# Kernel tuning notes

Hardware: AMD Instinct MI355X
Metric: run time of the kernel (lower is better)

The kernel has to match this reference:

```python
import jax, jax.numpy as jnp
import numpy as np

N1 = 50000; N2 = 50000; F = 256; HID = 64; H = 8; DH = HID // H; L = 2; E = 800000


def setup_inputs() -> dict:
    key = jax.random.key(0)
    ks = jax.random.split(key, 20)
    f32 = jnp.float32
    rn = lambda k, shape, s=0.1: jax.random.normal(k, shape, dtype=f32) * s
    inp = {}
    inp['x1'] = jax.random.normal(ks[0], (N1, F), dtype=f32)
    inp['x2'] = jax.random.normal(ks[1], (N2, F), dtype=f32)
    # row 0 = source node ids, row 1 = destination node ids
    inp['edge12'] = jax.random.randint(ks[2], (2, E), 0, N2)  # n1 -> n2
    inp['edge21'] = jax.random.randint(ks[3], (2, E), 0, N1)  # n2 -> n1
    inp['w_in'] = rn(ks[4], (2, HID, F))
    inp['b_in'] = rn(ks[5], (2, HID))
    inp['kw'] = rn(ks[6], (L, 2, HID, HID)); inp['kb'] = rn(ks[7], (L, 2, HID))
    inp['qw'] = rn(ks[8], (L, 2, HID, HID)); inp['qb'] = rn(ks[9], (L, 2, HID))
    inp['vw'] = rn(ks[10], (L, 2, HID, HID)); inp['vb'] = rn(ks[11], (L, 2, HID))
    inp['aw'] = rn(ks[12], (L, 2, HID, HID)); inp['ab'] = rn(ks[13], (L, 2, HID))
    inp['skip'] = jax.random.normal(ks[14], (L, 2), dtype=f32)
    inp['a_rel'] = rn(ks[15], (L, 2, H, DH, DH), 0.3)
    inp['m_rel'] = rn(ks[16], (L, 2, H, DH, DH), 0.3)
    inp['p_rel'] = jnp.ones((L, 2, H), dtype=f32)
    return inp


def _segment_softmax(logits, seg, n):
    # logits: [E, H], seg: [E] destination ids
    m = jax.ops.segment_max(logits, seg, num_segments=n)
    e = jnp.exp(logits - m[seg])
    s = jax.ops.segment_sum(e, seg, num_segments=n)
    return e / s[seg]


def reference(x1, x2, edge12, edge21, w_in, b_in, kw, kb, qw, qb, vw, vb, aw, ab,
              skip, a_rel, m_rel, p_rel):
    scale = jnp.asarray(1.0 / np.sqrt(DH), x1.dtype)

    def kqv(h, l, t):
        k = (h @ kw[l, t].T + kb[l, t]).reshape(-1, H, DH)
        q = (h @ qw[l, t].T + qb[l, t]).reshape(-1, H, DH)
        v = (h @ vw[l, t].T + vb[l, t]).reshape(-1, H, DH)
        return k, q, v

    def message(k_src, v_src, q_dst, edge, ar, mr, pr, n_dst):
        kr = jnp.einsum('nhd,hde->nhe', k_src, ar)   # per-node relation projection
        vr = jnp.einsum('nhd,hde->nhe', v_src, mr)
        s, d = edge[0], edge[1]
        logit = jnp.einsum('ehd,ehd->eh', q_dst[d], kr[s]) * pr[None, :] * scale
        alpha = _segment_softmax(logit, d, n_dst)     # [E, H]
        out = jax.ops.segment_sum(alpha[:, :, None] * vr[s], d, num_segments=n_dst)
        return out.reshape(n_dst, HID)

    def update(o, h, l, t):
        o = jax.nn.gelu(o, approximate=False) @ aw[l, t].T + ab[l, t]
        beta = jax.nn.sigmoid(skip[l, t])
        return beta * o + (1.0 - beta) * h

    # per-node-type input Linear + ReLU stem
    h1 = jax.nn.relu(x1 @ w_in[0].T + b_in[0])
    h2 = jax.nn.relu(x2 @ w_in[1].T + b_in[1])

    outs1, outs2 = [], []
    for l in range(L):
        k1, q1, v1 = kqv(h1, l, 0)
        k2, q2, v2 = kqv(h2, l, 1)
        o2 = message(k1, v1, q2, edge12, a_rel[l, 0], m_rel[l, 0], p_rel[l, 0], h2.shape[0])
        o1 = message(k2, v2, q1, edge21, a_rel[l, 1], m_rel[l, 1], p_rel[l, 1], h1.shape[0])
        h1 = update(o1, h1, l, 0)
        h2 = update(o2, h2, l, 1)
        outs1.append(h1)
        outs2.append(h2)

    Em = jnp.concatenate(outs1, axis=1)  # [N1, HID*L]
    Ed = jnp.concatenate(outs2, axis=1)  # [N2, HID*L]
    return Em, Ed
```

## Files before the change

### kernel.cpp

```cpp
#include <hip/hip_runtime.h>
#include <hip/hip_bf16.h>
#include <hip/hip_fp8.h>
#include <math.h>

typedef __attribute__((ext_vector_type(8))) short bf16x8;
typedef __attribute__((ext_vector_type(4))) float f32x4;
typedef __attribute__((ext_vector_type(4))) unsigned int u32x4;
typedef __attribute__((ext_vector_type(4))) int i32x4;
typedef unsigned short ushort_t;
typedef unsigned char uchar_t;

#define BUCKET_SHIFT 6
#define BUCKET_CAP   64

__device__ inline short f2b(float f) {
    __hip_bfloat16 h = __float2bfloat16(f);
    return __builtin_bit_cast(short, h);
}
__device__ inline float b2f(unsigned short u) {
    return __builtin_bit_cast(float, (unsigned int)u << 16);
}
__device__ inline float blo(unsigned int w) {
    return __builtin_bit_cast(float, w << 16);
}
__device__ inline float bhi(unsigned int w) {
    return __builtin_bit_cast(float, w & 0xffff0000u);
}
__device__ inline uchar_t f2f8(float f) {
    __hip_fp8_e4m3 h(f);
    return (uchar_t)h.__x;
}
__device__ inline float f82f(unsigned int u) {
    __hip_fp8_e4m3 h;
    h.__x = (__hip_fp8_storage_t)(u & 0xff);
    return (float)h;
}

__global__ __launch_bounds__(256) void prep_kernel(
    const float* __restrict__ w_in,
    const float* __restrict__ kw, const float* __restrict__ kb,
    const float* __restrict__ qw, const float* __restrict__ qb,
    const float* __restrict__ vw, const float* __restrict__ vb,
    const float* __restrict__ aw,
    const float* __restrict__ a_rel, const float* __restrict__ m_rel,
    const float* __restrict__ p_rel,
    short* __restrict__ wstem, short* __restrict__ Wcat,
    float* __restrict__ Bcat, short* __restrict__ Awb)
{
    int bid = blockIdx.x, tid = threadIdx.x;
    if (bid >= 4) {
        int t = bid - 4;
        for (int i = tid; i < 16384; i += 256)
            wstem[t * 16384 + i] = f2b(w_in[t * 16384 + i]);
        return;
    }
    int base = bid;
    const float* KW = kw + base * 4096;
    const float* QW = qw + base * 4096;
    const float* VW = vw + base * 4096;
    const float* AR = a_rel + base * 512;
    const float* MR = m_rel + base * 512;
    const float* PR = p_rel + base * 8;
    short* WC = Wcat + base * 12288;
    float* BC = Bcat + base * 192;

    for (int i = tid; i < 4096; i += 256) WC[i] = f2b(QW[i]);
    for (int i = tid; i < 4096; i += 256) {
        int out = i >> 6, in = i & 63;
        int h = out >> 3, e = out & 7;
        float s = PR[h] * 0.35355339059327373f;
        float acc = 0.f;
        #pragma unroll
        for (int d = 0; d < 8; ++d) acc += KW[(h * 8 + d) * 64 + in] * AR[h * 64 + d * 8 + e];
        WC[4096 + i] = f2b(acc * s);
    }
    for (int i = tid; i < 4096; i += 256) {
        int out = i >> 6, in = i & 63;
        int h = out >> 3, e = out & 7;
        float acc = 0.f;
        #pragma unroll
        for (int d = 0; d < 8; ++d) acc += VW[(h * 8 + d) * 64 + in] * MR[h * 64 + d * 8 + e];
        WC[8192 + i] = f2b(acc);
    }
    if (tid < 64) {
        BC[tid] = qb[base * 64 + tid];
    } else if (tid < 128) {
        int out = tid - 64;
        int h = out >> 3, e = out & 7;
        float s = PR[h] * 0.35355339059327373f;
        float acc = 0.f;
        #pragma unroll
        for (int d = 0; d < 8; ++d) acc += kb[base * 64 + h * 8 + d] * AR[h * 64 + d * 8 + e];
        BC[64 + out] = acc * s;
    } else if (tid < 192) {
        int out = tid - 128;
        int h = out >> 3, e = out & 7;
        float acc = 0.f;
        #pragma unroll
        for (int d = 0; d < 8; ++d) acc += vb[base * 64 + h * 8 + d] * MR[h * 64 + d * 8 + e];
        BC[128 + out] = acc;
    }
    for (int i = tid; i < 4096; i += 256) Awb[base * 4096 + i] = f2b(aw[base * 4096 + i]);
}

__global__ __launch_bounds__(256) void stem2_mfma(
    const float* __restrict__ X1, const float* __restrict__ X2,
    const short* __restrict__ Wb, const float* __restrict__ B1, const float* __restrict__ B2,
    short* __restrict__ H1, short* __restrict__ H2, int N1, int N2, int nt1)
{
    const float* X; const short* Wsrc; const float* B; short* Hb; int N; int tb;
    if (blockIdx.x < nt1) { X = X1; Wsrc = Wb;         B = B1; Hb = H1; N = N1; tb = blockIdx.x; }
    else                  { X = X2; Wsrc = Wb + 16384; B = B2; Hb = H2; N = N2; tb = blockIdx.x - nt1; }
    __shared__ short Ws[64 * 256];
    int tid = threadIdx.x;
    #pragma unroll
    for (int k = 0; k < 8; ++k) {
        int u = tid + k * 256;
        int row = u >> 5, c = u & 31;
        u32x4 v = *reinterpret_cast<const u32x4*>(Wsrc + row * 256 + c * 8);
        *reinterpret_cast<u32x4*>(&Ws[row * 256 + ((c ^ (row & 7)) << 3)]) = v;
    }
    __syncthreads();
    int w = tid >> 6, l = tid & 63;
    int g = l >> 4, q = l & 15;
    int row = tb * 64 + w * 16 + q;
    bool rok = row < N;
    f32x4 acc[4] = {};
    const float* xr = X + (size_t)row * 256 + g * 8;
    #pragma unroll
    for (int s = 0; s < 8; ++s) {
        bf16x8 a = {};
        if (rok) {
            float4 x0 = *reinterpret_cast<const float4*>(xr + s * 32);
            float4 x1 = *reinterpret_cast<const float4*>(xr + s * 32 + 4);
            a[0] = f2b(x0.x); a[1] = f2b(x0.y); a[2] = f2b(x0.z); a[3] = f2b(x0.w);
            a[4] = f2b(x1.x); a[5] = f2b(x1.y); a[6] = f2b(x1.z); a[7] = f2b(x1.w);
        }
        #pragma unroll
        for (int n = 0; n < 4; ++n) {
            int br = n * 16 + q;
            int c = s * 4 + g;
            bf16x8 b = *reinterpret_cast<bf16x8*>(&Ws[br * 256 + ((c ^ (br & 7)) << 3)]);
            acc[n] = __builtin_amdgcn_mfma_f32_16x16x32_bf16(a, b, acc[n], 0, 0, 0);
        }
    }
    int orow0 = tb * 64 + w * 16 + g * 4;
    #pragma unroll
    for (int n = 0; n < 4; ++n) {
        int col = n * 16 + q;
        float bias = B[col];
        #pragma unroll
        for (int r = 0; r < 4; ++r) {
            int orow = orow0 + r;
            if (orow < N)
                Hb[(size_t)orow * 64 + col] = f2b(fmaxf(acc[n][r] + bias, 0.f));
        }
    }
}

__global__ __launch_bounds__(256) void kqv2_mfma(
    const short* __restrict__ H1, const short* __restrict__ Wc1, const float* __restrict__ Bc1,
    short* __restrict__ Q1, uchar_t* __restrict__ KV1, int N1,
    const short* __restrict__ H2, const short* __restrict__ Wc2, const float* __restrict__ Bc2,
    short* __restrict__ Q2, uchar_t* __restrict__ KV2, int N2, int nt1)
{
    const short* Hb; const short* Wcat; const float* Bcat; short* Qb; uchar_t* KV; int N; int tb;
    if (blockIdx.x < nt1) { Hb = H1; Wcat = Wc1; Bcat = Bc1; Qb = Q1; KV = KV1; N = N1; tb = blockIdx.x; }
    else                  { Hb = H2; Wcat = Wc2; Bcat = Bc2; Qb = Q2; KV = KV2; N = N2; tb = blockIdx.x - nt1; }
    __shared__ short Ws[192 * 64];
    int tid = threadIdx.x;
    #pragma unroll
    for (int k = 0; k < 6; ++k) {
        int u = tid + k * 256;
        int row = u >> 3, c = u & 7;
        u32x4 v = *reinterpret_cast<const u32x4*>(Wcat + row * 64 + c * 8);
        *reinterpret_cast<u32x4*>(&Ws[row * 64 + ((c ^ (row & 7)) << 3)]) = v;
    }
    __syncthreads();
    int w = tid >> 6, l = tid & 63;
    int g = l >> 4, q = l & 15;
    int arow = tb * 64 + w * 16 + q;
    bool rok = arow < N;
    bf16x8 a0 = {}, a1 = {};
    if (rok) {
        a0 = *reinterpret_cast<const bf16x8*>(Hb + (size_t)arow * 64 + g * 8);
        a1 = *reinterpret_cast<const bf16x8*>(Hb + (size_t)arow * 64 + 32 + g * 8);
    }
    f32x4 acc[12] = {};
    #pragma unroll
    for (int n = 0; n < 12; ++n) {
        int br = n * 16 + q;
        bf16x8 b0 = *reinterpret_cast<bf16x8*>(&Ws[br * 64 + ((0 * 4 + g) ^ (br & 7)) * 8]);
        acc[n] = __builtin_amdgcn_mfma_f32_16x16x32_bf16(a0, b0, acc[n], 0, 0, 0);
        bf16x8 b1 = *reinterpret_cast<bf16x8*>(&Ws[br * 64 + ((1 * 4 + g) ^ (br & 7)) * 8]);
        acc[n] = __builtin_amdgcn_mfma_f32_16x16x32_bf16(a1, b1, acc[n], 0, 0, 0);
    }
    int orow0 = tb * 64 + w * 16 + g * 4;
    #pragma unroll
    for (int n = 0; n < 12; ++n) {
        int col = n * 16 + q;
        float bias = Bcat[col];
        #pragma unroll
        for (int r = 0; r < 4; ++r) {
            int orow = orow0 + r;
            if (orow < N) {
                float v = acc[n][r] + bias;
                if (n < 4)      Qb[(size_t)orow * 64 + col]              = f2b(v);
                else if (n < 8) KV[(size_t)orow * 128 + 2 * (col - 64)]  = f2f8(v);
                else            KV[(size_t)orow * 128 + 2 * (col - 128) + 1] = f2f8(v);
            }
        }
    }
}

__global__ __launch_bounds__(256) void bucket8d_kernel(
    const int* __restrict__ e12, const int* __restrict__ e21,
    int* __restrict__ cnt12, int* __restrict__ cnt21,
    ushort_t* __restrict__ cs12, ushort_t* __restrict__ cs21,
    int E, int N1, int N2, int G)
{
    int grp = blockIdx.x & 7;
    int blk = blockIdx.x >> 3;
    bool dirA = grp < 4;
    const int* srcp = dirA ? e12 : e21;
    const int* dstp = dirA ? (e12 + E) : (e21 + E);
    int* cnt = dirA ? cnt12 : cnt21;
    ushort_t* cs = dirA ? cs12 : cs21;
    int Nn = dirA ? N2 : N1;
    int qr = grp & 3;
    int range = (Nn + 3) >> 2;
    int lo = qr * range, hi = lo + range;
    int E4 = E >> 2;
    int stride = G * 256;
    for (int v = blk * 256 + threadIdx.x; v < E4; v += stride) {
        i32x4 d4 = __builtin_nontemporal_load(reinterpret_cast<const i32x4*>(dstp) + v);
        int base = v * 4;
        if (d4.x >= lo && d4.x < hi) { int p = atomicAdd(&cnt[d4.x], 1); if (p < BUCKET_CAP) cs[((size_t)d4.x << BUCKET_SHIFT) + p] = (ushort_t)srcp[base]; }
        if (d4.y >= lo && d4.y < hi) { int p = atomicAdd(&cnt[d4.y], 1); if (p < BUCKET_CAP) cs[((size_t)d4.y << BUCKET_SHIFT) + p] = (ushort_t)srcp[base + 1]; }
        if (d4.z >= lo && d4.z < hi) { int p = atomicAdd(&cnt[d4.z], 1); if (p < BUCKET_CAP) cs[((size_t)d4.z << BUCKET_SHIFT) + p] = (ushort_t)srcp[base + 2]; }
        if (d4.w >= lo && d4.w < hi) { int p = atomicAdd(&cnt[d4.w], 1); if (p < BUCKET_CAP) cs[((size_t)d4.w << BUCKET_SHIFT) + p] = (ushort_t)srcp[base + 3]; }
    }
    int tail = E & 3;
    if (blk == 0 && threadIdx.x < tail) {
        int i = E - tail + threadIdx.x;
        int d = dstp[i];
        if (d >= lo && d < hi) { int p = atomicAdd(&cnt[d], 1); if (p < BUCKET_CAP) cs[((size_t)d << BUCKET_SHIFT) + p] = (ushort_t)srcp[i]; }
    }
}

__global__ __launch_bounds__(256) void gather8_kernel(
    const int* __restrict__ cntA, const ushort_t* __restrict__ csA,
    const short* __restrict__ QA, const uchar_t* __restrict__ KVA, short* __restrict__ GA, int NA,
    const int* __restrict__ cntB, const ushort_t* __restrict__ csB,
    const short* __restrict__ QB, const uchar_t* __restrict__ KVB, short* __restrict__ GB, int NB)
{
    int grp = blockIdx.x & 7;
    int localBlock = (blockIdx.x >> 3) * 4 + (grp & 3);
    const int* cnt; const ushort_t* cs; const short* Qb; const uchar_t* KV; short* G; int N;
    if (grp < 4) { cnt = cntA; cs = csA; Qb = QA; KV = KVA; G = GA; N = NA; }
    else         { cnt = cntB; cs = csB; Qb = QB; KV = KVB; G = GB; N = NB; }
    int d = localBlock * 4 + (threadIdx.x >> 6);
    if (d >= N) return;
    int lane = threadIdx.x & 63;
    int j = lane & 15;
    int sub = lane >> 4;
    int deg = min(cnt[d], BUCKET_CAP);
    uint2 qw = *reinterpret_cast<const uint2*>(Qb + (size_t)d * 64 + 4 * j);
    float q0 = blo(qw.x), q1 = bhi(qw.x), q2 = blo(qw.y), q3 = bhi(qw.y);
    float a0 = 0.f, a1 = 0.f, a2 = 0.f, a3 = 0.f, den = 0.f;
    int idv = (lane < deg) ? (int)cs[((size_t)d << BUCKET_SHIFT) + lane] : 0;
    for (int i = 0; i < deg; i += 4) {
        int idx = i + sub;
        bool valid = idx < deg;
        int s = __shfl(idv, valid ? idx : 0);
        uint2 wv = *reinterpret_cast<const uint2*>(KV + (size_t)s * 128 + 8 * j);
        float k0 = f82f(wv.x),       v0 = f82f(wv.x >> 8);
        float k1 = f82f(wv.x >> 16), v1 = f82f(wv.x >> 24);
        float k2 = f82f(wv.y),       v2 = f82f(wv.y >> 8);
        float k3 = f82f(wv.y >> 16), v3 = f82f(wv.y >> 24);
        float t = q0 * k0;
        t = fmaf(q1, k1, t);
        t = fmaf(q2, k2, t);
        t = fmaf(q3, k3, t);
        t += __shfl_xor(t, 1);
        float e = valid ? __expf(t) : 0.f;
        den += e;
        a0 = fmaf(e, v0, a0);
        a1 = fmaf(e, v1, a1);
        a2 = fmaf(e, v2, a2);
        a3 = fmaf(e, v3, a3);
    }
    a0 += __shfl_xor(a0, 16); a1 += __shfl_xor(a1, 16);
    a2 += __shfl_xor(a2, 16); a3 += __shfl_xor(a3, 16);
    den += __shfl_xor(den, 16);
    a0 += __shfl_xor(a0, 32); a1 += __shfl_xor(a1, 32);
    a2 += __shfl_xor(a2, 32); a3 += __shfl_xor(a3, 32);
    den += __shfl_xor(den, 32);
    if (lane < 16) {
        float r = (den > 0.f) ? 1.f / den : 0.f;
        float o0 = a0 * r, o1 = a1 * r, o2 = a2 * r, o3 = a3 * r;
        float g0 = 0.5f * o0 * (1.f + erff(o0 * 0.70710678118654752f));
        float g1 = 0.5f * o1 * (1.f + erff(o1 * 0.70710678118654752f));
        float g2 = 0.5f * o2 * (1.f + erff(o2 * 0.70710678118654752f));
        float g3 = 0.5f * o3 * (1.f + erff(o3 * 0.70710678118654752f));
        uint2 pw;
        pw.x = ((unsigned int)(unsigned short)f2b(g0)) | (((unsigned int)(unsigned short)f2b(g1)) << 16);
        pw.y = ((unsigned int)(unsigned short)f2b(g2)) | (((unsigned int)(unsigned short)f2b(g3)) << 16);
        *reinterpret_cast<uint2*>(G + (size_t)d * 64 + 4 * j) = pw;
    }
}

__global__ __launch_bounds__(256) void updkqv_mfma(
    const short* __restrict__ G1, const short* __restrict__ Aw1, const float* __restrict__ Ab1,
    const float* __restrict__ sk1, short* __restrict__ H1, float* __restrict__ Out1, int N1,
    const short* __restrict__ G2, const short* __restrict__ Aw2, const float* __restrict__ Ab2,
    const float* __restrict__ sk2, short* __restrict__ H2, float* __restrict__ Out2, int N2,
    const short* __restrict__ Wc1n, const float* __restrict__ Bc1n,
    short* __restrict__ Q1, uchar_t* __restrict__ KV1,
    const short* __restrict__ Wc2n, const float* __restrict__ Bc2n,
    short* __restrict__ Q2, uchar_t* __restrict__ KV2,
    int nt1, int outColOff)
{
    const short* G; const short* Awb; const float* Ab; const float* skipp;
    short* Hb; float* Out; int N; int tb;
    const short* Wcat; const float* Bcat; short* Qb; uchar_t* KV;
    if (blockIdx.x < nt1) {
        G = G1; Awb = Aw1; Ab = Ab1; skipp = sk1; Hb = H1; Out = Out1; N = N1; tb = blockIdx.x;
        Wcat = Wc1n; Bcat = Bc1n; Qb = Q1; KV = KV1;
    } else {
        G = G2; Awb = Aw2; Ab = Ab2; skipp = sk2; Hb = H2; Out = Out2; N = N2; tb = blockIdx.x - nt1;
        Wcat = Wc2n; Bcat = Bc2n; Qb = Q2; KV = KV2;
    }
    __shared__ short Ws[192 * 64];
    __shared__ short hs[64][64];
    int tid = threadIdx.x;
    #pragma unroll
    for (int k = 0; k < 6; ++k) {
        int u = tid + k * 256;
        int row = u >> 3, c = u & 7;
        u32x4 v = *reinterpret_cast<const u32x4*>(Wcat + row * 64 + c * 8);
        *reinterpret_cast<u32x4*>(&Ws[row * 64 + ((c ^ (row & 7)) << 3)]) = v;
    }
    int w = tid >> 6, l = tid & 63;
    int g = l >> 4, q = l & 15;
    bf16x8 bfw[4][2];
    #pragma unroll
    for (int n = 0; n < 4; ++n)
        #pragma unroll
        for (int s = 0; s < 2; ++s)
            bfw[n][s] = *reinterpret_cast<const bf16x8*>(Awb + (n * 16 + q) * 64 + s * 32 + g * 8);
    float beta = 1.f / (1.f + __expf(-skipp[0]));
    int arow = tb * 64 + w * 16 + q;
    bool rok = arow < N;
    bf16x8 ua0 = {}, ua1 = {};
    if (rok) {
        ua0 = *reinterpret_cast<const bf16x8*>(G + (size_t)arow * 64 + g * 8);
        ua1 = *reinterpret_cast<const bf16x8*>(G + (size_t)arow * 64 + 32 + g * 8);
    }
    f32x4 uacc[4] = {};
    #pragma unroll
    for (int n = 0; n < 4; ++n) {
        uacc[n] = __builtin_amdgcn_mfma_f32_16x16x32_bf16(ua0, bfw[n][0], uacc[n], 0, 0, 0);
        uacc[n] = __builtin_amdgcn_mfma_f32_16x16x32_bf16(ua1, bfw[n][1], uacc[n], 0, 0, 0);
    }
    int orow0 = tb * 64 + w * 16 + g * 4;
    int lrow0 = w * 16 + g * 4;
    #pragma unroll
    for (int n = 0; n < 4; ++n) {
        int col = n * 16 + q;
        float bias = Ab[col];
        #pragma unroll
        for (int r = 0; r < 4; ++r) {
            int orow = orow0 + r;
            if (orow < N) {
                float hold = b2f(((const unsigned short*)Hb)[(size_t)orow * 64 + col]);
                float hnew = beta * (uacc[n][r] + bias) + (1.f - beta) * hold;
                short hb16 = f2b(hnew);
                Out[(size_t)orow * 128 + outColOff + col] = hnew;
                Hb[(size_t)orow * 64 + col] = hb16;
                hs[lrow0 + r][col] = hb16;
            } else {
                hs[lrow0 + r][col] = 0;
            }
        }
    }
    __syncthreads();
    bf16x8 a0 = *reinterpret_cast<const bf16x8*>(&hs[w * 16 + q][g * 8]);
    bf16x8 a1 = *reinterpret_cast<const bf16x8*>(&hs[w * 16 + q][32 + g * 8]);
    f32x4 acc[12] = {};
    #pragma unroll
    for (int n = 0; n < 12; ++n) {
        int br = n * 16 + q;
        bf16x8 b0 = *reinterpret_cast<bf16x8*>(&Ws[br * 64 + ((0 * 4 + g) ^ (br & 7)) * 8]);
        acc[n] = __builtin_amdgcn_mfma_f32_16x16x32_bf16(a0, b0, acc[n], 0, 0, 0);
        bf16x8 b1 = *reinterpret_cast<bf16x8*>(&Ws[br * 64 + ((1 * 4 + g) ^ (br & 7)) * 8]);
        acc[n] = __builtin_amdgcn_mfma_f32_16x16x32_bf16(a1, b1, acc[n], 0, 0, 0);
    }
    #pragma unroll
    for (int n = 0; n < 12; ++n) {
        int col = n * 16 + q;
        float bias = Bcat[col];
        #pragma unroll
        for (int r = 0; r < 4; ++r) {
            int orow = orow0 + r;
            if (orow < N) {
                float v = acc[n][r] + bias;
                if (n < 4)      Qb[(size_t)orow * 64 + col]              = f2b(v);
                else if (n < 8) KV[(size_t)orow * 128 + 2 * (col - 64)]  = f2f8(v);
                else            KV[(size_t)orow * 128 + 2 * (col - 128) + 1] = f2f8(v);
            }
        }
    }
}

__global__ __launch_bounds__(256) void update2_mfma(
    const short* __restrict__ G1, const short* __restrict__ Aw1, const float* __restrict__ Ab1,
    const float* __restrict__ sk1, short* __restrict__ H1, float* __restrict__ Out1, int N1,
    const short* __restrict__ G2, const short* __restrict__ Aw2, const float* __restrict__ Ab2,
    const float* __restrict__ sk2, short* __restrict__ H2, float* __restrict__ Out2, int N2,
    int nt1, int outColOff)
{
    const short* G; const short* Awb; const float* Ab; const float* skipp;
    short* Hb; float* Out; int N; int tb;
    if (blockIdx.x < nt1) { G = G1; Awb = Aw1; Ab = Ab1; skipp = sk1; Hb = H1; Out = Out1; N = N1; tb = blockIdx.x; }
    else                  { G = G2; Awb = Aw2; Ab = Ab2; skipp = sk2; Hb = H2; Out = Out2; N = N2; tb = blockIdx.x - nt1; }
    int tid = threadIdx.x;
    int w = tid >> 6, l = tid & 63;
    int g = l >> 4, q = l & 15;
    bf16x8 bf[4][2];
    #pragma unroll
    for (int n = 0; n < 4; ++n)
        #pragma unroll
        for (int s = 0; s < 2; ++s)
            bf[n][s] = *reinterpret_cast<const bf16x8*>(Awb + (n * 16 + q) * 64 + s * 32 + g * 8);
    float beta = 1.f / (1.f + __expf(-skipp[0]));
    int arow = tb * 64 + w * 16 + q;
    bool rok = arow < N;
    bf16x8 a0 = {}, a1 = {};
    if (rok) {
        a0 = *reinterpret_cast<const bf16x8*>(G + (size_t)arow * 64 + g * 8);
        a1 = *reinterpret_cast<const bf16x8*>(G + (size_t)arow * 64 + 32 + g * 8);
    }
    f32x4 acc[4] = {};
    #pragma unroll
    for (int n = 0; n < 4; ++n) {
        acc[n] = __builtin_amdgcn_mfma_f32_16x16x32_bf16(a0, bf[n][0], acc[n], 0, 0, 0);
        acc[n] = __builtin_amdgcn_mfma_f32_16x16x32_bf16(a1, bf[n][1], acc[n], 0, 0, 0);
    }
    int orow0 = tb * 64 + w * 16 + g * 4;
    #pragma unroll
    for (int n = 0; n < 4; ++n) {
        int col = n * 16 + q;
        float bias = Ab[col];
        #pragma unroll
        for (int r = 0; r < 4; ++r) {
            int orow = orow0 + r;
            if (orow < N) {
                float hold = b2f(((const unsigned short*)Hb)[(size_t)orow * 64 + col]);
                float hnew = beta * (acc[n][r] + bias) + (1.f - beta) * hold;
                Out[(size_t)orow * 128 + outColOff + col] = hnew;
                Hb[(size_t)orow * 64 + col] = f2b(hnew);
            }
        }
    }
}

extern "C" void kernel_launch(void* const* d_in, const int* in_sizes, int n_in,
                              void* d_out, int out_size, void* d_ws, size_t ws_size,
                              hipStream_t stream) {
    const float* x1    = (const float*)d_in[0];
    const float* x2    = (const float*)d_in[1];
    const int*   e12   = (const int*)d_in[2];
    const int*   e21   = (const int*)d_in[3];
    const float* w_in  = (const float*)d_in[4];
    const float* b_in  = (const float*)d_in[5];
    const float* kw    = (const float*)d_in[6];
    const float* kb    = (const float*)d_in[7];
    const float* qw    = (const float*)d_in[8];
    const float* qb    = (const float*)d_in[9];
    const float* vw    = (const float*)d_in[10];
    const float* vb    = (const float*)d_in[11];
    const float* aw    = (const float*)d_in[12];
    const float* ab    = (const float*)d_in[13];
    const float* skip  = (const float*)d_in[14];
    const float* a_rel = (const float*)d_in[15];
    const float* m_rel = (const float*)d_in[16];
    const float* p_rel = (const float*)d_in[17];

    int N1 = in_sizes[0] / 256;
    int N2 = in_sizes[1] / 256;
    int E  = in_sizes[2] / 2;

    float* out = (float*)d_out;

    char* wsp = (char*)d_ws;
    auto alloc = [&](size_t bytes) { void* p = wsp; wsp += (bytes + 255) & ~(size_t)255; return p; };
    short* hb1   = (short*)alloc((size_t)N1 * 64 * 2);
    short* hb2   = (short*)alloc((size_t)N2 * 64 * 2);
    short* qb1   = (short*)alloc((size_t)N1 * 64 * 2);
    short* qb2   = (short*)alloc((size_t)N2 * 64 * 2);
    uchar_t* kv1 = (uchar_t*)alloc((size_t)N1 * 128);
    uchar_t* kv2 = (uchar_t*)alloc((size_t)N2 * 128);
    short* g1    = (short*)alloc((size_t)N1 * 64 * 2);
    short* g2    = (short*)alloc((size_t)N2 * 64 * 2);
    short* wstem = (short*)alloc(2 * 16384 * 2);
    short* WcatB = (short*)alloc(4 * 12288 * 2);
    float* BcatB = (float*)alloc(4 * 192 * 4);
    short* AwbB  = (short*)alloc(4 * 4096 * 2);
    int* cnts    = (int*)alloc((size_t)(N1 + N2) * 4);
    int* cnt12   = cnts;
    int* cnt21   = cnts + N2;
    ushort_t* csr12 = (ushort_t*)alloc(((size_t)N2 << BUCKET_SHIFT) * 2);
    ushort_t* csr21 = (ushort_t*)alloc(((size_t)N1 << BUCKET_SHIFT) * 2);

    const int BLK = 256;
    int nt1 = (N1 + 63) / 64;
    int nt2 = (N2 + 63) / 64;
    const int G8 = 512;

    prep_kernel<<<6, BLK, 0, stream>>>(w_in, kw, kb, qw, qb, vw, vb, aw,
                                       a_rel, m_rel, p_rel, wstem, WcatB, BcatB, AwbB);

    hipMemsetAsync(cnts, 0, (size_t)(N1 + N2) * 4, stream);
    bucket8d_kernel<<<8 * G8, BLK, 0, stream>>>(e12, e21, cnt12, cnt21,
                                                csr12, csr21, E, N1, N2, G8);

    stem2_mfma<<<nt1 + nt2, BLK, 0, stream>>>(x1, x2, wstem, b_in, b_in + 64,
                                              hb1, hb2, N1, N2, nt1);

    int bA = (N2 + 3) / 4;
    int bB = (N1 + 3) / 4;
    int bmax = bA > bB ? bA : bB;
    int nlb = (bmax + 3) / 4;
    int gblocks = 8 * nlb;

    kqv2_mfma<<<nt1 + nt2, BLK, 0, stream>>>(
        hb1, WcatB + (size_t)0 * 12288, BcatB + (size_t)0 * 192, qb1, kv1, N1,
        hb2, WcatB + (size_t)1 * 12288, BcatB + (size_t)1 * 192, qb2, kv2, N2, nt1);

    gather8_kernel<<<gblocks, BLK, 0, stream>>>(
        cnt12, csr12, qb2, kv1, g2, N2,
        cnt21, csr21, qb1, kv2, g1, N1);

    updkqv_mfma<<<nt1 + nt2, BLK, 0, stream>>>(
        g1, AwbB + (size_t)0 * 4096, ab + (size_t)0 * 64, skip + 0, hb1, out, N1,
        g2, AwbB + (size_t)1 * 4096, ab + (size_t)1 * 64, skip + 1, hb2,
        out + (size_t)N1 * 128, N2,
        WcatB + (size_t)2 * 12288, BcatB + (size_t)2 * 192, qb1, kv1,
        WcatB + (size_t)3 * 12288, BcatB + (size_t)3 * 192, qb2, kv2,
        nt1, 0);

    gather8_kernel<<<gblocks, BLK, 0, stream>>>(
        cnt12, csr12, qb2, kv1, g2, N2,
        cnt21, csr21, qb1, kv2, g1, N1);

    update2_mfma<<<nt1 + nt2, BLK, 0, stream>>>(
        g1, AwbB + (size_t)2 * 4096, ab + (size_t)2 * 64, skip + 2, hb1, out, N1,
        g2, AwbB + (size_t)3 * 4096, ab + (size_t)3 * 64, skip + 3, hb2,
        out + (size_t)N1 * 128, N2, nt1, 64);
}
```

Before: 302.0 us.

## Replace global-atomic edge bucketing with two-level radix binning via shared-memory atomics

The single bucketing kernel, which ran global atomics per edge across four range-partitioned passes, is replaced by a four-kernel pipeline. It builds per-block histograms of 64-node bins in LDS, scans them in a single block, scatters packed (local dst, src) payloads into bin order, and then expands each bin into the fixed-capacity per-node source lists in shared memory. This removes contended global atomics and scattered 2-byte writes, and it also drops the memset. The cost is extra kernel launches, a serial single-block scan, and an extra round trip through a payload buffer of E words per direction.

After: 353.2 us. +17.0%, slower.

```diff
diff --git a/kernel.cpp b/kernel.cpp
--- a/kernel.cpp
+++ b/kernel.cpp
@@ -12,6 +12,7 @@
 
 #define BUCKET_SHIFT 6
 #define BUCKET_CAP   64
+#define SB_ 32
 
 __device__ inline short f2b(float f) {
     __hip_bfloat16 h = __float2bfloat16(f);
@@ -213,39 +214,165 @@
     }
 }
 
-__global__ __launch_bounds__(256) void bucket8d_kernel(
+__global__ __launch_bounds__(256) void radix_hist(
     const int* __restrict__ e12, const int* __restrict__ e21,
-    int* __restrict__ cnt12, int* __restrict__ cnt21,
-    ushort_t* __restrict__ cs12, ushort_t* __restrict__ cs21,
-    int E, int N1, int N2, int G)
-{
-    int grp = blockIdx.x & 7;
-    int blk = blockIdx.x >> 3;
-    bool dirA = grp < 4;
+    int* __restrict__ histA, int* __restrict__ histB,
+    int E, int nbA, int nbB)
+{
+    int blk = blockIdx.x;
+    bool dirA = blk < SB_;
+    int b = dirA ? blk : blk - SB_;
+    const int* dstp = dirA ? (e12 + E) : (e21 + E);
+    int nb = dirA ? nbA : nbB;
+    int* hist = dirA ? histA : histB;
+    __shared__ int h[1024];
+    for (int i = threadIdx.x; i < nb; i += 256) h[i] = 0;
+    __syncthreads();
+    int EV = E >> 2;
+    int vchunk = (EV + SB_ - 1) / SB_;
+    int vs = b * vchunk, ve = min(EV, vs + vchunk);
+    for (int v = vs + threadIdx.x; v < ve; v += 256) {
+        i32x4 d4 = __builtin_nontemporal_load(reinterpret_cast<const i32x4*>(dstp) + v);
+        atomicAdd(&h[d4.x >> 6], 1);
+        atomicAdd(&h[d4.y >> 6], 1);
+        atomicAdd(&h[d4.z >> 6], 1);
+        atomicAdd(&h[d4.w >> 6], 1);
+    }
+    if (b == 0) {
+        int tail = E & 3;
+        if ((int)threadIdx.x < tail) {
+            int d = dstp[E - tail + threadIdx.x];
+            atomicAdd(&h[d >> 6], 1);
+        }
+    }
+    __syncthreads();
+    for (int i = threadIdx.x; i < nb; i += 256) hist[b * nb + i] = h[i];
+}
+
+__global__ __launch_bounds__(256) void radix_scan(
+    const int* __restrict__ histA, const int* __restrict__ histB,
+    int* __restrict__ offA, int* __restrict__ offB,
+    int* __restrict__ bsA, int* __restrict__ bsB, int nbA, int nbB)
+{
+    __shared__ int tsum[256];
+    int tid = threadIdx.x;
+    for (int dir = 0; dir < 2; ++dir) {
+        const int* hist = dir ? histB : histA;
+        int* off = dir ? offB : offA;
+        int* bs = dir ? bsB : bsA;
+        int nb = dir ? nbB : nbA;
+        int per = (nb + 255) >> 8;
+        int b0 = tid * per;
+        int loc[8];
+        int lsum = 0;
+        for (int k = 0; k < per; ++k) {
+            int b = b0 + k;
+            int t = 0;
+            if (b < nb)
+                for (int r = 0; r < SB_; ++r) t += hist[r * nb + b];
+            loc[k] = t; lsum += t;
+        }
+        __syncthreads();
+        tsum[tid] = lsum;
+        __syncthreads();
+        for (int ofs = 1; ofs < 256; ofs <<= 1) {
+            int v = (tid >= ofs) ? tsum[tid - ofs] : 0;
+            __syncthreads();
+            tsum[tid] += v;
+            __syncthreads();
+        }
+        int run = tid ? tsum[tid - 1] : 0;
+        for (int k = 0; k < per; ++k) {
+            int b = b0 + k;
+            if (b < nb) {
+                bs[b] = run;
+                int r2 = run;
+                for (int r = 0; r < SB_; ++r) {
+                    off[r * nb + b] = r2;
+                    r2 += hist[r * nb + b];
+                }
+            }
+            run += loc[k];
+        }
+        if (tid == 255) bs[nb] = tsum[255];
+        __syncthreads();
+    }
+}
+
+__global__ __launch_bounds__(256) void radix_scatter(
+    const int* __restrict__ e12, const int* __restrict__ e21,
+    const int* __restrict__ offA, const int* __restrict__ offB,
+    unsigned int* __restrict__ payA, unsigned int* __restrict__ payB,
+    int E, int nbA, int nbB)
+{
+    int blk = blockIdx.x;
+    bool dirA = blk < SB_;
+    int b = dirA ? blk : blk - SB_;
     const int* srcp = dirA ? e12 : e21;
     const int* dstp = dirA ? (e12 + E) : (e21 + E);
+    const int* off = dirA ? offA : offB;
+    unsigned int* pay = dirA ? payA : payB;
+    int nb = dirA ? nbA : nbB;
+    __shared__ int offs[1024];
+    for (int i = threadIdx.x; i < nb; i += 256) offs[i] = off[b * nb + i];
+    __syncthreads();
+    int EV = E >> 2;
+    int vchunk = (EV + SB_ - 1) / SB_;
+    int vs = b * vchunk, ve = min(EV, vs + vchunk);
+    for (int v = vs + threadIdx.x; v < ve; v += 256) {
+        i32x4 d4 = __builtin_nontemporal_load(reinterpret_cast<const i32x4*>(dstp) + v);
+        i32x4 s4 = __builtin_nontemporal_load(reinterpret_cast<const i32x4*>(srcp) + v);
+        int p;
+        p = atomicAdd(&offs[d4.x >> 6], 1); pay[p] = (((unsigned int)(d4.x & 63)) << 16) | (unsigned int)s4.x;
+        p = atomicAdd(&offs[d4.y >> 6], 1); pay[p] = (((unsigned int)(d4.y & 63)) << 16) | (unsigned int)s4.y;
+        p = atomicAdd(&offs[d4.z >> 6], 1); pay[p] = (((unsigned int)(d4.z & 63)) << 16) | (unsigned int)s4.z;
+        p = atomicAdd(&offs[d4.w >> 6], 1); pay[p] = (((unsigned int)(d4.w & 63)) << 16) | (unsigned int)s4.w;
+    }
+    if (b == 0) {
+        int tail = E & 3;
+        if ((int)threadIdx.x < tail) {
+            int i = E - tail + threadIdx.x;
+            int d = dstp[i];
+            int p = atomicAdd(&offs[d >> 6], 1);
+            pay[p] = (((unsigned int)(d & 63)) << 16) | (unsigned int)srcp[i];
+        }
+    }
+}
+
+__global__ __launch_bounds__(256) void bin_expand(
+    const unsigned int* __restrict__ payA, const int* __restrict__ bsA, int nbA,
+    ushort_t* __restrict__ cs12, int* __restrict__ cnt12, int NdA,
+    const unsigned int* __restrict__ payB, const int* __restrict__ bsB, int nbB,
+    ushort_t* __restrict__ cs21, int* __restrict__ cnt21, int NdB)
+{
+    int blk = blockIdx.x;
+    bool dirA = blk < nbA;
+    int b = dirA ? blk : blk - nbA;
+    const unsigned int* pay = dirA ? payA : payB;
+    const int* bs = dirA ? bsA : bsB;
+    ushort_t* cs = dirA ? cs12 : cs21;
     int* cnt = dirA ? cnt12 : cnt21;
-    ushort_t* cs = dirA ? cs12 : cs21;
-    int Nn = dirA ? N2 : N1;
-    int qr = grp & 3;
-    int range = (Nn + 3) >> 2;
-    int lo = qr * range, hi = lo + range;
-    int E4 = E >> 2;
-    int stride = G * 256;
-    for (int v = blk * 256 + threadIdx.x; v < E4; v += stride) {
-        i32x4 d4 = __builtin_nontemporal_load(reinterpret_cast<const i32x4*>(dstp) + v);
-        int base = v * 4;
-        if (d4.x >= lo && d4.x < hi) { int p = atomicAdd(&cnt[d4.x], 1); if (p < BUCKET_CAP) cs[((size_t)d4.x << BUCKET_SHIFT) + p] = (ushort_t)srcp[base]; }
-        if (d4.y >= lo && d4.y < hi) { int p = atomicAdd(&cnt[d4.y], 1); if (p < BUCKET_CAP) cs[((size_t)d4.y << BUCKET_SHIFT) + p] = (ushort_t)srcp[base + 1]; }
-        if (d4.z >= lo && d4.z < hi) { int p = atomicAdd(&cnt[d4.z], 1); if (p < BUCKET_CAP) cs[((size_t)d4.z << BUCKET_SHIFT) + p] = (ushort_t)srcp[base + 2]; }
-        if (d4.w >= lo && d4.w < hi) { int p = atomicAdd(&cnt[d4.w], 1); if (p < BUCKET_CAP) cs[((size_t)d4.w << BUCKET_SHIFT) + p] = (ushort_t)srcp[base + 3]; }
-    }
-    int tail = E & 3;
-    if (blk == 0 && threadIdx.x < tail) {
-        int i = E - tail + threadIdx.x;
-        int d = dstp[i];
-        if (d >= lo && d < hi) { int p = atomicAdd(&cnt[d], 1); if (p < BUCKET_CAP) cs[((size_t)d << BUCKET_SHIFT) + p] = (ushort_t)srcp[i]; }
-    }
+    int Nd = dirA ? NdA : NdB;
+    __shared__ int c[64];
+    __shared__ ushort_t list[64 * 64];
+    if (threadIdx.x < 64) c[threadIdx.x] = 0;
+    __syncthreads();
+    int rs = bs[b], re = bs[b + 1];
+    for (int i = rs + threadIdx.x; i < re; i += 256) {
+        unsigned int e = pay[i];
+        int dl = e >> 16;
+        int pos = atomicAdd(&c[dl], 1);
+        if (pos < BUCKET_CAP) list[(dl << 6) + pos] = (ushort_t)(e & 0xffff);
+    }
+    __syncthreads();
+    int d0 = b << 6;
+    int nrow = min(64, Nd - d0);
+    if (nrow <= 0) return;
+    const unsigned int* lsrc = reinterpret_cast<const unsigned int*>(list);
+    unsigned int* gdst = reinterpret_cast<unsigned int*>(cs + ((size_t)d0 << 6));
+    int nu32 = nrow << 5;
+    for (int u = threadIdx.x; u < nu32; u += 256) gdst[u] = lsrc[u];
+    if ((int)threadIdx.x < nrow) cnt[d0 + threadIdx.x] = c[threadIdx.x];
 }
 
 __global__ __launch_bounds__(256) void gather8_kernel(
@@ -507,23 +634,34 @@
     short* WcatB = (short*)alloc(4 * 12288 * 2);
     float* BcatB = (float*)alloc(4 * 192 * 4);
     short* AwbB  = (short*)alloc(4 * 4096 * 2);
-    int* cnts    = (int*)alloc((size_t)(N1 + N2) * 4);
-    int* cnt12   = cnts;
-    int* cnt21   = cnts + N2;
+    int* cnt12   = (int*)alloc((size_t)N2 * 4);
+    int* cnt21   = (int*)alloc((size_t)N1 * 4);
     ushort_t* csr12 = (ushort_t*)alloc(((size_t)N2 << BUCKET_SHIFT) * 2);
     ushort_t* csr21 = (ushort_t*)alloc(((size_t)N1 << BUCKET_SHIFT) * 2);
+
+    int nbA = (N2 + 63) >> 6;
+    int nbB = (N1 + 63) >> 6;
+    int* histA = (int*)alloc((size_t)SB_ * nbA * 4);
+    int* histB = (int*)alloc((size_t)SB_ * nbB * 4);
+    int* offA  = (int*)alloc((size_t)SB_ * nbA * 4);
+    int* offB  = (int*)alloc((size_t)SB_ * nbB * 4);
+    int* bsA   = (int*)alloc((size_t)(nbA + 1) * 4);
+    int* bsB   = (int*)alloc((size_t)(nbB + 1) * 4);
+    unsigned int* payA = (unsigned int*)alloc((size_t)E * 4);
+    unsigned int* payB = (unsigned int*)alloc((size_t)E * 4);
 
     const int BLK = 256;
     int nt1 = (N1 + 63) / 64;
     int nt2 = (N2 + 63) / 64;
-    const int G8 = 512;
 
     prep_kernel<<<6, BLK, 0, stream>>>(w_in, kw, kb, qw, qb, vw, vb, aw,
                                        a_rel, m_rel, p_rel, wstem, WcatB, BcatB, AwbB);
 
-    hipMemsetAsync(cnts, 0, (size_t)(N1 + N2) * 4, stream);
-    bucket8d_kernel<<<8 * G8, BLK, 0, stream>>>(e12, e21, cnt12, cnt21,
-                                                csr12, csr21, E, N1, N2, G8);
+    radix_hist<<<2 * SB_, BLK, 0, stream>>>(e12, e21, histA, histB, E, nbA, nbB);
+    radix_scan<<<1, BLK, 0, stream>>>(histA, histB, offA, offB, bsA, bsB, nbA, nbB);
+    radix_scatter<<<2 * SB_, BLK, 0, stream>>>(e12, e21, offA, offB, payA, payB, E, nbA, nbB);
+    bin_expand<<<nbA + nbB, BLK, 0, stream>>>(payA, bsA, nbA, csr12, cnt12, N2,
+                                              payB, bsB, nbB, csr21, cnt21, N1);
 
     stem2_mfma<<<nt1 + nt2, BLK, 0, stream>>>(x1, x2, wstem, b_in, b_in + 64,
                                               hb1, hb2, N1, N2, nt1);
```
